# Optimization experiments

Measured on AMD Instinct MI355X. Metric: run time of the kernel, lower is better.

The kernel has to match this reference:

```python
import jax, jax.numpy as jnp
import numpy as np

BLOCKSIZE = 64  # elements per quantization block


def setup_inputs() -> dict:
    key = jax.random.key(0)
    k1, k2, k3, k4 = jax.random.split(key, 4)
    out_features, in_features = 11008, 4096
    tokens = 8192  # batch 4 * seq 2048
    n = out_features * in_features
    x = jax.random.normal(k1, (tokens, in_features), dtype=jnp.float32)
    codes = jax.random.randint(k2, (n,), 0, 16, dtype=jnp.int32)
    absmax = jax.random.uniform(k3, (n // BLOCKSIZE,), dtype=jnp.float32)
    # NF4-style codebook (16 quantization levels)
    codebook = jnp.array(
        [-1.0, -0.6962, -0.5251, -0.3949, -0.2844, -0.1848, -0.0911, 0.0,
         0.0796, 0.1609, 0.2461, 0.3379, 0.4407, 0.5626, 0.7230, 1.0],
        dtype=jnp.float32)
    bias = jax.random.normal(k4, (out_features,), dtype=jnp.float32)
    return {"x": x, "codes": codes, "absmax": absmax,
            "codebook": codebook, "bias": bias}


def reference(x, codes, absmax, codebook, bias):
    out_features, in_features = 11008, 4096
    # Dequantize: codebook lookup, then per-block scale.  [n] -> [out, in]
    w = codebook[codes].reshape(-1, BLOCKSIZE) * absmax[:, None]
    w = w.reshape(out_features, in_features)
    # y = x @ W.T + b
    y = jnp.einsum('ti,oi->to', x, w) + bias
    return y
```

## Files before the change

### kernel.cpp

```cpp
#include <hip/hip_runtime.h>
#include <hip/hip_bf16.h>
#include <stdint.h>

#define TOKENS 8192
#define OUTF   11008
#define INF    4096
#define NCODES (45088768)

typedef __bf16 bf16x8 __attribute__((ext_vector_type(8)));
typedef float  f32x4  __attribute__((ext_vector_type(4)));

__device__ __forceinline__ unsigned short f32_to_bf16_rne(float f) {
    union { float f; unsigned int u; } v; v.f = f;
    unsigned int u = v.u;
    unsigned int r = u + 0x7fffu + ((u >> 16) & 1u);
    return (unsigned short)(r >> 16);
}

__global__ __launch_bounds__(256) void dequant_w(const int* __restrict__ codes,
                                                 const float* __restrict__ absmax,
                                                 const float* __restrict__ codebook,
                                                 unsigned short* __restrict__ wq) {
    __shared__ float cb[16];
    if (threadIdx.x < 16) cb[threadIdx.x] = codebook[threadIdx.x];
    __syncthreads();
    size_t idx = ((size_t)blockIdx.x * 256 + threadIdx.x) * 8;
    float am = absmax[idx >> 6];
    const int4* cp = (const int4*)(codes + idx);
    int4 c0 = cp[0];
    int4 c1 = cp[1];
    union { unsigned short s[8]; uint4 v; } u;
    u.s[0] = f32_to_bf16_rne(cb[c0.x] * am);
    u.s[1] = f32_to_bf16_rne(cb[c0.y] * am);
    u.s[2] = f32_to_bf16_rne(cb[c0.z] * am);
    u.s[3] = f32_to_bf16_rne(cb[c0.w] * am);
    u.s[4] = f32_to_bf16_rne(cb[c1.x] * am);
    u.s[5] = f32_to_bf16_rne(cb[c1.y] * am);
    u.s[6] = f32_to_bf16_rne(cb[c1.z] * am);
    u.s[7] = f32_to_bf16_rne(cb[c1.w] * am);
    *(uint4*)(wq + idx) = u.v;
}

__global__ __launch_bounds__(256) void cast_x(const float* __restrict__ x,
                                              unsigned short* __restrict__ xq) {
    size_t idx = ((size_t)blockIdx.x * 256 + threadIdx.x) * 8;
    float4 a = *(const float4*)(x + idx);
    float4 b = *(const float4*)(x + idx + 4);
    union { unsigned short s[8]; uint4 v; } u;
    u.s[0] = f32_to_bf16_rne(a.x);
    u.s[1] = f32_to_bf16_rne(a.y);
    u.s[2] = f32_to_bf16_rne(a.z);
    u.s[3] = f32_to_bf16_rne(a.w);
    u.s[4] = f32_to_bf16_rne(b.x);
    u.s[5] = f32_to_bf16_rne(b.y);
    u.s[6] = f32_to_bf16_rne(b.z);
    u.s[7] = f32_to_bf16_rne(b.w);
    *(uint4*)(xq + idx) = u.v;
}

#define BM 256
#define BN 256
#define BK 64

#define GLLDS(SRC, DST)                                                                   \
    __builtin_amdgcn_global_load_lds((const __attribute__((address_space(1))) void*)(SRC),\
                                     (__attribute__((address_space(3))) void*)(DST), 16, 0, 0)

#define STAGE_A(KT, HALF, BUF) do {                                                       \
    const unsigned short* _s = gA + (size_t)(HALF) * (128 * INF) + (size_t)(KT) * BK;     \
    GLLDS(_s,                   &lA[BUF][(HALF) * 8192 + tid * 8]);                       \
    GLLDS(_s + (size_t)64 * INF, &lA[BUF][(HALF) * 8192 + tid * 8 + 4096]); } while (0)

#define STAGE_B(KT, HALF, BUF) do {                                                       \
    const unsigned short* _s = gB + (size_t)(HALF) * (128 * INF) + (size_t)(KT) * BK;     \
    GLLDS(_s,                   &lB[BUF][(HALF) * 8192 + tid * 8]);                       \
    GLLDS(_s + (size_t)64 * INF, &lB[BUF][(HALF) * 8192 + tid * 8 + 4096]); } while (0)

#define LOAD_A(BUF, MH) do { _Pragma("unroll")                                            \
    for (int i = 0; i < 4; ++i) {                                                         \
        a[i][0] = *(const bf16x8*)&lA[BUF][(MH) * 8192 + i * 1024 + aRow + sw0];          \
        a[i][1] = *(const bf16x8*)&lA[BUF][(MH) * 8192 + i * 1024 + aRow + sw1]; } } while (0)

#define LOAD_BX(BUF, NH, DST) do { _Pragma("unroll")                                      \
    for (int j = 0; j < 2; ++j) {                                                         \
        DST[j][0] = *(const bf16x8*)&lB[BUF][(NH) * 8192 + j * 1024 + bRow + sw0];        \
        DST[j][1] = *(const bf16x8*)&lB[BUF][(NH) * 8192 + j * 1024 + bRow + sw1]; } } while (0)

#define MFMA_Q(MH, NH, BSRC) do {                                                         \
    __builtin_amdgcn_s_setprio(1);                                                        \
    _Pragma("unroll") for (int kc = 0; kc < 2; ++kc)                                      \
    _Pragma("unroll") for (int i = 0; i < 4; ++i)                                         \
    _Pragma("unroll") for (int j = 0; j < 2; ++j)                                         \
        acc[MH][i][NH][j] = __builtin_amdgcn_mfma_f32_16x16x32_bf16(                      \
            a[i][kc], BSRC[j][kc], acc[MH][i][NH][j], 0, 0, 0);                           \
    __builtin_amdgcn_s_setprio(0); } while (0)

#define BARR   __builtin_amdgcn_s_barrier()
#define LGKM0  asm volatile("s_waitcnt lgkmcnt(0)" ::: "memory")
#define VMC(N) asm volatile("s_waitcnt vmcnt(" #N ")" ::: "memory")

__global__ __launch_bounds__(512, 2) void gemm_bf16_8p(const unsigned short* __restrict__ Xb,
                                                       const unsigned short* __restrict__ Wb,
                                                       const float* __restrict__ bias,
                                                       float* __restrict__ out) {
    __shared__ __align__(16) unsigned short lA[2][BM * BK];
    __shared__ __align__(16) unsigned short lB[2][BN * BK];

    const int bid  = blockIdx.x;
    const int xcd  = bid & 7;
    const int loc  = bid >> 3;
    const int mt   = xcd * 4 + (loc & 3);
    const int nt   = loc >> 2;
    const int m0   = mt * BM;
    const int n0   = nt * BN;

    const int tid  = threadIdx.x;
    const int lane = tid & 63;
    const int wave = tid >> 6;
    const int wm_l = wave >> 2;
    const int wn_l = wave & 3;

    const int frow = lane & 15;
    const int klan = lane >> 4;
    const int f7   = lane & 7;
    const int sw0  = ((klan)     ^ f7) * 8;
    const int sw1  = ((klan + 4) ^ f7) * 8;
    const int aRow = (wm_l * 64 + frow) * BK;
    const int bRow = (wn_l * 32 + frow) * BK;

    const int rl   = tid >> 3;
    const int gsw  = (tid & 7) ^ (rl & 7);
    const unsigned short* gA = Xb + (size_t)(m0 + rl) * INF + gsw * 8;
    const unsigned short* gB = Wb + (size_t)(n0 + rl) * INF + gsw * 8;

    f32x4 acc[2][4][2][2];
#pragma unroll
    for (int mh = 0; mh < 2; ++mh)
#pragma unroll
        for (int i = 0; i < 4; ++i)
#pragma unroll
            for (int nh = 0; nh < 2; ++nh)
#pragma unroll
                for (int j = 0; j < 2; ++j)
#pragma unroll
                    for (int r = 0; r < 4; ++r) acc[mh][i][nh][j][r] = 0.0f;

    bf16x8 a[4][2], bA[2][2], bB[2][2];

    STAGE_A(0, 0, 0); STAGE_B(0, 1, 0); STAGE_A(0, 1, 0); STAGE_B(0, 0, 0);
    STAGE_A(1, 0, 1); STAGE_B(1, 1, 1); STAGE_A(1, 1, 1);
    VMC(6);
    BARR;

    for (int it = 0; it < 31; ++it) {
        const int kt1 = 2 * it + 1, kt2 = 2 * it + 2, kt3 = 2 * it + 3;
        LOAD_A(0, 0); LOAD_BX(0, 0, bA); STAGE_B(kt1, 0, 1);
        BARR; LGKM0; MFMA_Q(0, 0, bA); BARR;
        LOAD_BX(0, 1, bB); STAGE_A(kt2, 0, 0);
        BARR; LGKM0; MFMA_Q(0, 1, bB); BARR;
        LOAD_A(0, 1); STAGE_B(kt2, 1, 0);
        BARR; LGKM0; MFMA_Q(1, 1, bB); BARR;
        STAGE_A(kt2, 1, 0);
        BARR; LGKM0; MFMA_Q(1, 0, bA); VMC(6); BARR;
        LOAD_A(1, 0); LOAD_BX(1, 0, bA); STAGE_B(kt2, 0, 0);
        BARR; LGKM0; MFMA_Q(0, 0, bA); BARR;
        LOAD_BX(1, 1, bB); STAGE_A(kt3, 0, 1);
        BARR; LGKM0; MFMA_Q(0, 1, bB); BARR;
        LOAD_A(1, 1); STAGE_B(kt3, 1, 1);
        BARR; LGKM0; MFMA_Q(1, 1, bB); BARR;
        STAGE_A(kt3, 1, 1);
        BARR; LGKM0; MFMA_Q(1, 0, bA); VMC(6); BARR;
    }

    LOAD_A(0, 0); LOAD_BX(0, 0, bA); STAGE_B(63, 0, 1);
    BARR; LGKM0; MFMA_Q(0, 0, bA); BARR;
    LOAD_BX(0, 1, bB);
    BARR; LGKM0; MFMA_Q(0, 1, bB); BARR;
    LOAD_A(0, 1);
    BARR; LGKM0; MFMA_Q(1, 1, bB); BARR;
    BARR; LGKM0; MFMA_Q(1, 0, bA); VMC(0); BARR;
    LOAD_A(1, 0); LOAD_BX(1, 0, bA);
    BARR; LGKM0; MFMA_Q(0, 0, bA); BARR;
    LOAD_BX(1, 1, bB);
    BARR; LGKM0; MFMA_Q(0, 1, bB); BARR;
    LOAD_A(1, 1);
    BARR; LGKM0; MFMA_Q(1, 1, bB); BARR;
    LGKM0; MFMA_Q(1, 0, bA);

    const int crow = (lane >> 4) * 4;
    const int ccol = lane & 15;
#pragma unroll
    for (int mh = 0; mh < 2; ++mh)
#pragma unroll
        for (int nh = 0; nh < 2; ++nh)
#pragma unroll
            for (int j = 0; j < 2; ++j) {
                const int n = n0 + nh * 128 + wn_l * 32 + j * 16 + ccol;
                const float bv = bias[n];
#pragma unroll
                for (int i = 0; i < 4; ++i) {
                    const int m = m0 + mh * 128 + wm_l * 64 + i * 16 + crow;
#pragma unroll
                    for (int r = 0; r < 4; ++r) {
                        const float v = acc[mh][i][nh][j][r] + bv;
                        __builtin_nontemporal_store(v, &out[(size_t)(m + r) * OUTF + n]);
                    }
                }
            }
}

__global__ __launch_bounds__(256) void fused_fallback(const float* __restrict__ x,
                                                      const int* __restrict__ codes,
                                                      const float* __restrict__ absmax,
                                                      const float* __restrict__ codebook,
                                                      const float* __restrict__ bias,
                                                      float* __restrict__ out) {
    __shared__ float xs[64][17];
    __shared__ float wsm[64][17];
    __shared__ float cb[16];
    const int tid = threadIdx.x;
    if (tid < 16) cb[tid] = codebook[tid];
    const int m0 = blockIdx.y * 64, n0 = blockIdx.x * 64;
    float acc[4][4] = {};
    const int tr = tid >> 4, tc = tid & 15;
    for (int k0 = 0; k0 < INF; k0 += 16) {
        __syncthreads();
#pragma unroll
        for (int i = 0; i < 4; i++) {
            int e = i * 256 + tid;
            int r = e >> 4, c = e & 15;
            xs[r][c] = x[(size_t)(m0 + r) * INF + k0 + c];
            size_t widx = (size_t)(n0 + r) * INF + k0 + c;
            wsm[r][c] = cb[codes[widx]] * absmax[widx >> 6];
        }
        __syncthreads();
#pragma unroll
        for (int kk = 0; kk < 16; kk++) {
            float xv[4], wv[4];
#pragma unroll
            for (int i = 0; i < 4; i++) xv[i] = xs[tr * 4 + i][kk];
#pragma unroll
            for (int j = 0; j < 4; j++) wv[j] = wsm[tc * 4 + j][kk];
#pragma unroll
            for (int i = 0; i < 4; i++)
#pragma unroll
                for (int j = 0; j < 4; j++) acc[i][j] += xv[i] * wv[j];
        }
    }
#pragma unroll
    for (int i = 0; i < 4; i++)
#pragma unroll
        for (int j = 0; j < 4; j++) {
            int m = m0 + tr * 4 + i, n = n0 + tc * 4 + j;
            out[(size_t)m * OUTF + n] = acc[i][j] + bias[n];
        }
}

extern "C" void kernel_launch(void* const* d_in, const int* in_sizes, int n_in,
                              void* d_out, int out_size, void* d_ws, size_t ws_size,
                              hipStream_t stream) {
    const float* x        = (const float*)d_in[0];
    const int*   codes    = (const int*)d_in[1];
    const float* absmax   = (const float*)d_in[2];
    const float* codebook = (const float*)d_in[3];
    const float* bias     = (const float*)d_in[4];
    float* out = (float*)d_out;

    const size_t wbytes = (size_t)NCODES * 2;
    const size_t xbytes = (size_t)TOKENS * INF * 2;

    if (ws_size >= wbytes + xbytes) {
        unsigned short* wq = (unsigned short*)d_ws;
        unsigned short* xq = (unsigned short*)((char*)d_ws + wbytes);
        dequant_w<<<NCODES / 2048, 256, 0, stream>>>(codes, absmax, codebook, wq);
        cast_x<<<(TOKENS * INF) / 2048, 256, 0, stream>>>(x, xq);
        gemm_bf16_8p<<<dim3((TOKENS / BM) * (OUTF / BN)), 512, 0, stream>>>(xq, wq, bias, out);
    } else {
        dim3 grid(OUTF / 64, TOKENS / 64);
        fused_fallback<<<grid, 64 * 4, 0, stream>>>(x, codes, absmax, codebook, bias, out);
    }
}
```

Before: 1.248 ms.

## Double-buffer LDS fragment registers to overlap reads with MFMA quadrants

Restructures the GEMM main loop so each phase issues the LDS fragment reads for the next quadrant into a second register set while running MFMAs on the current one. Barriers and staging are reordered, with sched_barrier keeping the reads ahead of the MFMAs, and one barrier per phase is dropped. The goal is to hide LDS read latency behind matrix math and remove the lgkmcnt stalls before each MFMA block. It raises register pressure, since two A/B fragment sets are live, and it makes the barrier and vmcnt ordering more delicate around buffer reuse.

```diff
diff --git a/kernel.cpp b/kernel.cpp
--- a/kernel.cpp
+++ b/kernel.cpp
@@ -76,28 +76,28 @@
     GLLDS(_s,                   &lB[BUF][(HALF) * 8192 + tid * 8]);                       \
     GLLDS(_s + (size_t)64 * INF, &lB[BUF][(HALF) * 8192 + tid * 8 + 4096]); } while (0)
 
-#define LOAD_A(BUF, MH) do { _Pragma("unroll")                                            \
-    for (int i = 0; i < 4; ++i) {                                                         \
-        a[i][0] = *(const bf16x8*)&lA[BUF][(MH) * 8192 + i * 1024 + aRow + sw0];          \
-        a[i][1] = *(const bf16x8*)&lA[BUF][(MH) * 8192 + i * 1024 + aRow + sw1]; } } while (0)
-
-#define LOAD_BX(BUF, NH, DST) do { _Pragma("unroll")                                      \
-    for (int j = 0; j < 2; ++j) {                                                         \
-        DST[j][0] = *(const bf16x8*)&lB[BUF][(NH) * 8192 + j * 1024 + bRow + sw0];        \
-        DST[j][1] = *(const bf16x8*)&lB[BUF][(NH) * 8192 + j * 1024 + bRow + sw1]; } } while (0)
-
-#define MFMA_Q(MH, NH, BSRC) do {                                                         \
+#define READS(AD, BD, BUF, MH, NH) do {                                                   \
+    _Pragma("unroll") for (int i = 0; i < 4; ++i) {                                       \
+        AD[i][0] = *(const bf16x8*)&lA[BUF][(MH) * 8192 + i * 1024 + aRow + sw0];         \
+        AD[i][1] = *(const bf16x8*)&lA[BUF][(MH) * 8192 + i * 1024 + aRow + sw1]; }       \
+    _Pragma("unroll") for (int j = 0; j < 2; ++j) {                                       \
+        BD[j][0] = *(const bf16x8*)&lB[BUF][(NH) * 8192 + j * 1024 + bRow + sw0];         \
+        BD[j][1] = *(const bf16x8*)&lB[BUF][(NH) * 8192 + j * 1024 + bRow + sw1]; } } while (0)
+
+#define MFMA_Q(AS, BS, MH, NH) do {                                                       \
     __builtin_amdgcn_s_setprio(1);                                                        \
     _Pragma("unroll") for (int kc = 0; kc < 2; ++kc)                                      \
     _Pragma("unroll") for (int i = 0; i < 4; ++i)                                         \
     _Pragma("unroll") for (int j = 0; j < 2; ++j)                                         \
         acc[MH][i][NH][j] = __builtin_amdgcn_mfma_f32_16x16x32_bf16(                      \
-            a[i][kc], BSRC[j][kc], acc[MH][i][NH][j], 0, 0, 0);                           \
+            AS[i][kc], BS[j][kc], acc[MH][i][NH][j], 0, 0, 0);                            \
     __builtin_amdgcn_s_setprio(0); } while (0)
 
-#define BARR   __builtin_amdgcn_s_barrier()
+#define BARRM  do { asm volatile("" ::: "memory"); __builtin_amdgcn_s_barrier();          \
+                    asm volatile("" ::: "memory"); } while (0)
 #define LGKM0  asm volatile("s_waitcnt lgkmcnt(0)" ::: "memory")
 #define VMC(N) asm volatile("s_waitcnt vmcnt(" #N ")" ::: "memory")
+#define SCHED0 __builtin_amdgcn_sched_barrier(0)
 
 __global__ __launch_bounds__(512, 2) void gemm_bf16_8p(const unsigned short* __restrict__ Xb,
                                                        const unsigned short* __restrict__ Wb,
@@ -145,47 +145,37 @@
 #pragma unroll
                     for (int r = 0; r < 4; ++r) acc[mh][i][nh][j][r] = 0.0f;
 
-    bf16x8 a[4][2], bA[2][2], bB[2][2];
+    bf16x8 a0[4][2], b0[2][2];
+    bf16x8 a1[4][2], b1[2][2];
 
     STAGE_A(0, 0, 0); STAGE_B(0, 1, 0); STAGE_A(0, 1, 0); STAGE_B(0, 0, 0);
-    STAGE_A(1, 0, 1); STAGE_B(1, 1, 1); STAGE_A(1, 1, 1);
-    VMC(6);
-    BARR;
+    STAGE_A(1, 0, 1); STAGE_B(1, 1, 1);
+    VMC(4);
+    BARRM;
+    READS(a0, b0, 0, 0, 0);
 
     for (int it = 0; it < 31; ++it) {
         const int kt1 = 2 * it + 1, kt2 = 2 * it + 2, kt3 = 2 * it + 3;
-        LOAD_A(0, 0); LOAD_BX(0, 0, bA); STAGE_B(kt1, 0, 1);
-        BARR; LGKM0; MFMA_Q(0, 0, bA); BARR;
-        LOAD_BX(0, 1, bB); STAGE_A(kt2, 0, 0);
-        BARR; LGKM0; MFMA_Q(0, 1, bB); BARR;
-        LOAD_A(0, 1); STAGE_B(kt2, 1, 0);
-        BARR; LGKM0; MFMA_Q(1, 1, bB); BARR;
-        STAGE_A(kt2, 1, 0);
-        BARR; LGKM0; MFMA_Q(1, 0, bA); VMC(6); BARR;
-        LOAD_A(1, 0); LOAD_BX(1, 0, bA); STAGE_B(kt2, 0, 0);
-        BARR; LGKM0; MFMA_Q(0, 0, bA); BARR;
-        LOAD_BX(1, 1, bB); STAGE_A(kt3, 0, 1);
-        BARR; LGKM0; MFMA_Q(0, 1, bB); BARR;
-        LOAD_A(1, 1); STAGE_B(kt3, 1, 1);
-        BARR; LGKM0; MFMA_Q(1, 1, bB); BARR;
-        STAGE_A(kt3, 1, 1);
-        BARR; LGKM0; MFMA_Q(1, 0, bA); VMC(6); BARR;
+        BARRM; LGKM0; STAGE_A(kt1, 1, 1); READS(a1, b1, 0, 0, 1); SCHED0; MFMA_Q(a0, b0, 0, 0);
+        BARRM; LGKM0; STAGE_B(kt1, 0, 1); READS(a0, b0, 0, 1, 1); SCHED0; MFMA_Q(a1, b1, 0, 1);
+        BARRM; LGKM0; STAGE_A(kt2, 0, 0); READS(a1, b1, 0, 1, 0); SCHED0; MFMA_Q(a0, b0, 1, 1);
+        BARRM; LGKM0; VMC(2); BARRM;
+        STAGE_B(kt2, 1, 0); READS(a0, b0, 1, 0, 0); SCHED0; MFMA_Q(a1, b1, 1, 0);
+        BARRM; LGKM0; STAGE_A(kt2, 1, 0); READS(a1, b1, 1, 0, 1); SCHED0; MFMA_Q(a0, b0, 0, 0);
+        BARRM; LGKM0; STAGE_B(kt2, 0, 0); READS(a0, b0, 1, 1, 1); SCHED0; MFMA_Q(a1, b1, 0, 1);
+        BARRM; LGKM0; STAGE_A(kt3, 0, 1); READS(a1, b1, 1, 1, 0); SCHED0; MFMA_Q(a0, b0, 1, 1);
+        BARRM; LGKM0; VMC(2); BARRM;
+        STAGE_B(kt3, 1, 1); READS(a0, b0, 0, 0, 0); SCHED0; MFMA_Q(a1, b1, 1, 0);
     }
 
-    LOAD_A(0, 0); LOAD_BX(0, 0, bA); STAGE_B(63, 0, 1);
-    BARR; LGKM0; MFMA_Q(0, 0, bA); BARR;
-    LOAD_BX(0, 1, bB);
-    BARR; LGKM0; MFMA_Q(0, 1, bB); BARR;
-    LOAD_A(0, 1);
-    BARR; LGKM0; MFMA_Q(1, 1, bB); BARR;
-    BARR; LGKM0; MFMA_Q(1, 0, bA); VMC(0); BARR;
-    LOAD_A(1, 0); LOAD_BX(1, 0, bA);
-    BARR; LGKM0; MFMA_Q(0, 0, bA); BARR;
-    LOAD_BX(1, 1, bB);
-    BARR; LGKM0; MFMA_Q(0, 1, bB); BARR;
-    LOAD_A(1, 1);
-    BARR; LGKM0; MFMA_Q(1, 1, bB); BARR;
-    LGKM0; MFMA_Q(1, 0, bA);
+    BARRM; LGKM0; STAGE_A(63, 1, 1); READS(a1, b1, 0, 0, 1); SCHED0; MFMA_Q(a0, b0, 0, 0);
+    BARRM; LGKM0; STAGE_B(63, 0, 1); READS(a0, b0, 0, 1, 1); SCHED0; MFMA_Q(a1, b1, 0, 1);
+    BARRM; LGKM0;                    READS(a1, b1, 0, 1, 0); SCHED0; MFMA_Q(a0, b0, 1, 1);
+    BARRM; LGKM0; VMC(0); BARRM;     READS(a0, b0, 1, 0, 0); SCHED0; MFMA_Q(a1, b1, 1, 0);
+    BARRM; LGKM0;                    READS(a1, b1, 1, 0, 1); SCHED0; MFMA_Q(a0, b0, 0, 0);
+    BARRM; LGKM0;                    READS(a0, b0, 1, 1, 1); SCHED0; MFMA_Q(a1, b1, 0, 1);
+    BARRM; LGKM0;                    READS(a1, b1, 1, 1, 0); SCHED0; MFMA_Q(a0, b0, 1, 1);
+    BARRM; LGKM0;                                            SCHED0; MFMA_Q(a1, b1, 1, 0);
 
     const int crow = (lane >> 4) * 4;
     const int ccol = lane & 15;
@@ -277,6 +267,6 @@
         gemm_bf16_8p<<<dim3((TOKENS / BM) * (OUTF / BN)), 512, 0, stream>>>(xq, wq, bias, out);
     } else {
         dim3 grid(OUTF / 64, TOKENS / 64);
-        fused_fallback<<<grid, 64 * 4, 0, stream>>>(x, codes, absmax, codebook, bias, out);
+        fused_fallback<<<grid, 256, 0, stream>>>(x, codes, absmax, codebook, bias, out);
     }
 }
```

Measured after the change: 1.423 ms. +14.0%, slower.
